# Kernel optimization log

Hardware: AMD Instinct MI355X
Metric: run time of the kernel (lower is better)

## Reference

```python
import jax, jax.numpy as jnp
import numpy as np

B, SQ, SKV, D = 4, 2048, 2048, 768
H, HD = 12, 16  # num_heads, reduced head_dim (64 / reduce_factor 4)
DR = H * HD     # 192 reduced width


def setup_inputs() -> dict:
    key = jax.random.key(0)
    ks = jax.random.split(key, 6)
    s = 0.02
    return {
        "hidden_states": jax.random.normal(ks[0], (B, SQ, D), jnp.float32),
        "encoder_hidden_states": jax.random.normal(ks[1], (B, SKV, D), jnp.float32),
        "Wq": jax.random.normal(ks[2], (D, DR), jnp.float32) * s,
        "bq": jnp.zeros((DR,), jnp.float32),
        "Wkv": jax.random.normal(ks[3], (D, 2 * DR), jnp.float32) * s,
        "bkv": jnp.zeros((2 * DR,), jnp.float32),
        "Wp": jax.random.normal(ks[4], (DR, D), jnp.float32) * s,
        "bp": jnp.zeros((D,), jnp.float32),
    }


def _split_heads(x):
    # [B, S, DR] -> [B, H, S, HD]
    b, s, _ = x.shape
    return x.reshape(b, s, H, HD).transpose(0, 2, 1, 3)


def reference(hidden_states, encoder_hidden_states, Wq, bq, Wkv, bkv, Wp, bp):
    # Conv1D projections (x @ W + b)
    q = hidden_states @ Wq + bq                       # [B, SQ, 192]
    kv = encoder_hidden_states @ Wkv + bkv            # [B, SKV, 384]
    k, v = kv[..., :DR], kv[..., DR:]
    q = _split_heads(q)                               # [B, H, SQ, HD]
    k = _split_heads(k)                               # [B, H, SKV, HD]
    v = _split_heads(v)                               # [B, H, SKV, HD]
    scale = jnp.asarray(HD, q.dtype) ** 0.5
    scores = jnp.einsum('bhqd,bhkd->bhqk', q, k) / scale
    attn = jax.nn.softmax(scores, axis=-1)            # dropout is identity in eval
    out = jnp.einsum('bhqk,bhkd->bhqd', attn, v)      # [B, H, SQ, HD]
    out = out.transpose(0, 2, 1, 3).reshape(hidden_states.shape[0], -1, DR)
    out = out @ Wp + bp                               # [B, SQ, 768]
    return out
```

## Files before the change

kernel.cpp:

```cpp
#include <hip/hip_runtime.h>
#include <hip/hip_bf16.h>
#include <math.h>

#define NB 4
#define NSQ 2048
#define NSKV 2048
#define ND 768
#define NH 12
#define NHD 16
#define NDR 192
#define M_TOT (NB * NSQ)

typedef __attribute__((ext_vector_type(8)))  short          bf16x8;
typedef __attribute__((ext_vector_type(16))) float          f32x16;
typedef __attribute__((ext_vector_type(8)))  unsigned short u16x8;

__device__ __forceinline__ unsigned short bfbits(float x) {
  __hip_bfloat16 h = __float2bfloat16(x);
  unsigned short u; __builtin_memcpy(&u, &h, 2); return u;
}
__device__ __forceinline__ float bf2f(unsigned short u) {
  unsigned int v = ((unsigned int)u) << 16; float f; __builtin_memcpy(&f, &v, 4); return f;
}
__device__ __forceinline__ unsigned int pk2t(float a, float b) {
  unsigned int ua, ub;
  __builtin_memcpy(&ua, &a, 4); __builtin_memcpy(&ub, &b, 4);
#if __has_builtin(__builtin_amdgcn_perm)
  return __builtin_amdgcn_perm(ub, ua, 0x07060302);
#else
  return (ua >> 16) | (ub & 0xffff0000u);
#endif
}
__device__ __forceinline__ float exp2_raw(float x) {
#if __has_builtin(__builtin_amdgcn_exp2f)
  return __builtin_amdgcn_exp2f(x);
#else
  float r; asm("v_exp_f32 %0, %1" : "=v"(r) : "v"(x)); return r;
#endif
}
__device__ __forceinline__ void g2l16(const void* g, void* l) {
  __builtin_amdgcn_global_load_lds(
      (const __attribute__((address_space(1))) void*)g,
      (__attribute__((address_space(3))) void*)l, 16, 0, 0);
}

#define QSCALE 0.36067376022224085f
#define LDSBUF 16384

__global__ __launch_bounds__(256) void prep(
    const float* __restrict__ Wq, const float* __restrict__ Wkv,
    const float* __restrict__ Wp,
    unsigned short* __restrict__ WSq, unsigned short* __restrict__ WSkv,
    unsigned short* __restrict__ WSp) {
  int bid = blockIdx.x;
  const float* W; unsigned short* out; int Nn, KBLK, bx, by;
  if (bid < 72)        { W = Wq;  out = WSq;  Nn = 192; KBLK = 24; bx = bid % 24;        by = bid / 24; }
  else if (bid < 216)  { int b = bid - 72;  W = Wkv; out = WSkv; Nn = 384; KBLK = 24; bx = b % 24; by = b / 24; }
  else                 { int b = bid - 216; W = Wp;  out = WSp;  Nn = 768; KBLK = 6;  bx = b % 6;  by = b / 6;  }

  __shared__ float tile[32][65];
  int k0 = bx * 32, n0 = by * 64;
  int t = threadIdx.x;
  int kr = t >> 3, c0 = (t & 7) * 8;
  const float* src = W + (size_t)(k0 + kr) * Nn + n0 + c0;
  float4 f0 = *reinterpret_cast<const float4*>(src);
  float4 f1 = *reinterpret_cast<const float4*>(src + 4);
  tile[kr][c0+0] = f0.x; tile[kr][c0+1] = f0.y; tile[kr][c0+2] = f0.z; tile[kr][c0+3] = f0.w;
  tile[kr][c0+4] = f1.x; tile[kr][c0+5] = f1.y; tile[kr][c0+6] = f1.z; tile[kr][c0+7] = f1.w;
  __syncthreads();
  int n = t >> 2, cq0 = (t & 3) * 2;
  int ng = n0 + n, sw = ng & 7;
  unsigned short* dst = out + ((size_t)ng * KBLK + bx) * 64;
  #pragma unroll
  for (int q = 0; q < 2; ++q) {
    int cc = cq0 + q;
    u16x8 v;
    #pragma unroll
    for (int i = 0; i < 8; ++i) {
      float x = tile[(cc & 3) * 8 + i][n];
      unsigned short h = bfbits(x);
      v[i] = (cc < 4) ? h : bfbits(x - bf2f(h));
    }
    *reinterpret_cast<u16x8*>(dst + (cc ^ sw) * 8) = v;
  }
}

__device__ __forceinline__ void core_compute(
    const unsigned short* const (&ard)[4], const unsigned short* const (&wrd)[12],
    int off, f32x16 (&acc)[3]) {
  #pragma unroll
  for (int kk = 0; kk < 2; ++kk) {
    bf16x8 ah = *reinterpret_cast<const bf16x8*>(ard[kk*2+0] + off);
    bf16x8 al = *reinterpret_cast<const bf16x8*>(ard[kk*2+1] + off);
    #pragma unroll
    for (int nr = 0; nr < 3; ++nr) {
      bf16x8 wh = *reinterpret_cast<const bf16x8*>(wrd[(nr*2+kk)*2+0] + off);
      bf16x8 wl = *reinterpret_cast<const bf16x8*>(wrd[(nr*2+kk)*2+1] + off);
      acc[nr] = __builtin_amdgcn_mfma_f32_32x32x16_bf16(ah, wh, acc[nr], 0, 0, 0);
      acc[nr] = __builtin_amdgcn_mfma_f32_32x32x16_bf16(ah, wl, acc[nr], 0, 0, 0);
      acc[nr] = __builtin_amdgcn_mfma_f32_32x32x16_bf16(al, wh, acc[nr], 0, 0, 0);
    }
  }
}

__device__ __forceinline__ void gemm_core(
    const unsigned short* __restrict__ As,
    const unsigned short* __restrict__ Ws,
    const float* __restrict__ bias,
    int KBLK, unsigned short* lds, f32x16 (&acc)[3]) {
  const int tid = threadIdx.x;
  const int wv = tid >> 6, lane = tid & 63;
  const int l31 = lane & 31, hi8 = lane >> 5;
  const int wm = wv >> 1, wn = wv & 1;

  unsigned short* Ab = lds;
  unsigned short* Wb = lds + 64 * 64;

  const int r8 = lane >> 3, c8 = lane & 7;
  const size_t rowu = (size_t)KBLK * 64;

  const unsigned short* srcA0 = As + (size_t)((0*4 + wv)*8 + r8) * rowu + c8*8;
  const unsigned short* srcA1 = As + (size_t)((1*4 + wv)*8 + r8) * rowu + c8*8;
  const unsigned short* srcW[6];
  #pragma unroll
  for (int j = 0; j < 6; ++j)
    srcW[j] = Ws + (size_t)((j*4 + wv)*8 + r8) * rowu + c8*8;

  unsigned short* dA0 = Ab + ((0*4 + wv)*64 + lane) * 8;
  unsigned short* dA1 = Ab + ((1*4 + wv)*64 + lane) * 8;
  unsigned short* dW[6];
  #pragma unroll
  for (int j = 0; j < 6; ++j)
    dW[j] = Wb + ((j*4 + wv)*64 + lane) * 8;

  const int ra = wm*32 + l31;
  const unsigned short* ard[4];
  #pragma unroll
  for (int kk = 0; kk < 2; ++kk) {
    ard[kk*2+0] = Ab + ra*64 + (((kk*2 + hi8)     ^ (ra & 7)) * 8);
    ard[kk*2+1] = Ab + ra*64 + (((4 + kk*2 + hi8) ^ (ra & 7)) * 8);
  }
  const unsigned short* wrd[12];
  #pragma unroll
  for (int nr = 0; nr < 3; ++nr) {
    int rw = wn*96 + nr*32 + l31;
    #pragma unroll
    for (int kk = 0; kk < 2; ++kk) {
      wrd[(nr*2+kk)*2+0] = Wb + rw*64 + (((kk*2 + hi8)     ^ (rw & 7)) * 8);
      wrd[(nr*2+kk)*2+1] = Wb + rw*64 + (((4 + kk*2 + hi8) ^ (rw & 7)) * 8);
    }
  }

  #pragma unroll
  for (int nr = 0; nr < 3; ++nr) {
    float bv = bias[wn*96 + nr*32 + l31];
    #pragma unroll
    for (int r = 0; r < 16; ++r) acc[nr][r] = bv;
  }

  g2l16(srcA0, dA0); srcA0 += 64;
  g2l16(srcA1, dA1); srcA1 += 64;
  #pragma unroll
  for (int j = 0; j < 6; ++j) { g2l16(srcW[j], dW[j]); srcW[j] += 64; }
  __syncthreads();

  for (int kb = 0; kb < KBLK; kb += 2) {
    if (kb + 1 < KBLK) {
      g2l16(srcA0, dA0 + LDSBUF); srcA0 += 64;
      g2l16(srcA1, dA1 + LDSBUF); srcA1 += 64;
      #pragma unroll
      for (int j = 0; j < 6; ++j) { g2l16(srcW[j], dW[j] + LDSBUF); srcW[j] += 64; }
    }
    core_compute(ard, wrd, 0, acc);
    __syncthreads();
    if (kb + 2 < KBLK) {
      g2l16(srcA0, dA0); srcA0 += 64;
      g2l16(srcA1, dA1); srcA1 += 64;
      #pragma unroll
      for (int j = 0; j < 6; ++j) { g2l16(srcW[j], dW[j]); srcW[j] += 64; }
    }
    core_compute(ard, wrd, LDSBUF, acc);
    __syncthreads();
  }
}

#define QHALF 10240
__global__ __launch_bounds__(384) void gemm_qkv(
    const float* __restrict__ A1, const float* __restrict__ A2,
    const unsigned short* __restrict__ WSq, const unsigned short* __restrict__ WSkv,
    const float* __restrict__ bq, const float* __restrict__ bkv,
    unsigned short* __restrict__ Qbf, unsigned short* __restrict__ Kbf,
    unsigned short* __restrict__ VTbf) {
  __shared__ unsigned short lds[2 * QHALF];
  const int bid = blockIdx.x;
  const float* Afp; const unsigned short* Ws; const float* bias;
  int m0, mode, ntile;
  if (bid < 256) {
    mode = 0; ntile = (bid & 1) * 96;
    Afp = A1; Ws = WSq + (size_t)ntile * (24*64); bias = bq + ntile;
    m0 = (bid >> 1) * 64;
  } else {
    int b2 = bid - 256;
    int sub = b2 & 3;
    m0 = (b2 >> 2) * 64;
    Afp = A2;
    if (sub < 2) { mode = 1; ntile = sub * 96;
                   Ws = WSkv + (size_t)ntile * (24*64); bias = bkv + ntile; }
    else         { mode = 2; ntile = (sub - 2) * 96;
                   Ws = WSkv + (size_t)(192 + ntile) * (24*64); bias = bkv + 192 + ntile; }
  }
  Afp += (size_t)m0 * ND;

  const int tid = threadIdx.x;
  const int wv = tid >> 6, lane = tid & 63;
  const int l31 = lane & 31, hi8 = lane >> 5;
  const int wm = wv & 1, wn = wv >> 1;

  unsigned short* Ab = lds;
  unsigned short* Wb = lds + 64*64;

  const int ar = tid >> 2, cq = tid & 3;
  const bool doA = (tid < 256);
  const float* srcA = Afp + (size_t)(doA ? ar : 0) * ND + cq*8;
  unsigned short* dAh = Ab + (doA ? ar : 0)*64 + ((cq       ^ (ar & 7)) * 8);
  unsigned short* dAl = Ab + (doA ? ar : 0)*64 + (((cq + 4) ^ (ar & 7)) * 8);

  const int wch0 = tid, wch1 = tid + 384;
  const unsigned short* srcW0 = Ws + (size_t)(wch0 >> 3) * (24*64) + (wch0 & 7) * 8;
  const unsigned short* srcW1 = Ws + (size_t)(wch1 >> 3) * (24*64) + (wch1 & 7) * 8;
  unsigned short* dW0 = Wb + wch0 * 8;
  unsigned short* dW1 = Wb + wch1 * 8;

  const int ra = wm*32 + l31;
  const int rw = wn*32 + l31;
  const unsigned short* ard[4];
  const unsigned short* wrd[4];
  #pragma unroll
  for (int kk = 0; kk < 2; ++kk) {
    ard[kk*2+0] = Ab + ra*64 + (((kk*2 + hi8)     ^ (ra & 7)) * 8);
    ard[kk*2+1] = Ab + ra*64 + (((4 + kk*2 + hi8) ^ (ra & 7)) * 8);
    wrd[kk*2+0] = Wb + rw*64 + (((kk*2 + hi8)     ^ (rw & 7)) * 8);
    wrd[kk*2+1] = Wb + rw*64 + (((4 + kk*2 + hi8) ^ (rw & 7)) * 8);
  }

  f32x16 acc;
  {
    float bv = bias[wn*32 + l31];
    #pragma unroll
    for (int r = 0; r < 16; ++r) acc[r] = bv;
  }

  {
    g2l16(srcW0, dW0); srcW0 += 64;
    g2l16(srcW1, dW1); srcW1 += 64;
    if (doA) {
      float4 f0 = *reinterpret_cast<const float4*>(srcA);
      float4 f1 = *reinterpret_cast<const float4*>(srcA + 4);
      float x[8] = {f0.x, f0.y, f0.z, f0.w, f1.x, f1.y, f1.z, f1.w};
      u16x8 hv, lv;
      #pragma unroll
      for (int i = 0; i < 8; ++i) {
        unsigned short h = bfbits(x[i]);
        hv[i] = h; lv[i] = bfbits(x[i] - bf2f(h));
      }
      *reinterpret_cast<u16x8*>(dAh) = hv;
      *reinterpret_cast<u16x8*>(dAl) = lv;
    }
    srcA += 32;
  }
  __syncthreads();

  #define QKV_COMPUTE(off)                                                     \
    {                                                                          \
      _Pragma("unroll")                                                        \
      for (int kk = 0; kk < 2; ++kk) {                                         \
        bf16x8 ah = *reinterpret_cast<const bf16x8*>(ard[kk*2+0] + (off));     \
        bf16x8 al = *reinterpret_cast<const bf16x8*>(ard[kk*2+1] + (off));     \
        bf16x8 wh = *reinterpret_cast<const bf16x8*>(wrd[kk*2+0] + (off));     \
        bf16x8 wl = *reinterpret_cast<const bf16x8*>(wrd[kk*2+1] + (off));     \
        acc = __builtin_amdgcn_mfma_f32_32x32x16_bf16(ah, wh, acc, 0, 0, 0);   \
        acc = __builtin_amdgcn_mfma_f32_32x32x16_bf16(ah, wl, acc, 0, 0, 0);   \
        acc = __builtin_amdgcn_mfma_f32_32x32x16_bf16(al, wh, acc, 0, 0, 0);   \
      }                                                                        \
    }

  for (int kb = 0; kb < 24; kb += 2) {
    float4 f0, f1;
    g2l16(srcW0, dW0 + QHALF); srcW0 += 64;
    g2l16(srcW1, dW1 + QHALF); srcW1 += 64;
    if (doA) {
      f0 = *reinterpret_cast<const float4*>(srcA);
      f1 = *reinterpret_cast<const float4*>(srcA + 4);
    }
    srcA += 32;
    QKV_COMPUTE(0)
    if (doA) {
      float x[8] = {f0.x, f0.y, f0.z, f0.w, f1.x, f1.y, f1.z, f1.w};
      u16x8 hv, lv;
      #pragma unroll
      for (int i = 0; i < 8; ++i) {
        unsigned short h = bfbits(x[i]);
        hv[i] = h; lv[i] = bfbits(x[i] - bf2f(h));
      }
      *reinterpret_cast<u16x8*>(dAh + QHALF) = hv;
      *reinterpret_cast<u16x8*>(dAl + QHALF) = lv;
    }
    __syncthreads();
    bool has2 = (kb + 2 < 24);
    if (has2) {
      g2l16(srcW0, dW0); srcW0 += 64;
      g2l16(srcW1, dW1); srcW1 += 64;
      if (doA) {
        f0 = *reinterpret_cast<const float4*>(srcA);
        f1 = *reinterpret_cast<const float4*>(srcA + 4);
      }
      srcA += 32;
    }
    QKV_COMPUTE(QHALF)
    if (has2 && doA) {
      float x[8] = {f0.x, f0.y, f0.z, f0.w, f1.x, f1.y, f1.z, f1.w};
      u16x8 hv, lv;
      #pragma unroll
      for (int i = 0; i < 8; ++i) {
        unsigned short h = bfbits(x[i]);
        hv[i] = h; lv[i] = bfbits(x[i] - bf2f(h));
      }
      *reinterpret_cast<u16x8*>(dAh) = hv;
      *reinterpret_cast<u16x8*>(dAl) = lv;
    }
    __syncthreads();
  }
  #undef QKV_COMPUTE

  if (mode == 2) {
    unsigned short (*tile)[65] = reinterpret_cast<unsigned short(*)[65]>(lds);
    #pragma unroll
    for (int r = 0; r < 16; ++r) {
      int key_l = wm*32 + (r & 3) + 8*(r >> 2) + 4*hi8;
      tile[wn*32 + l31][key_l] = bfbits(acc[r]);
    }
    __syncthreads();
    int b = m0 >> 11, key0 = m0 & 2047;
    #pragma unroll
    for (int j = 0; j < 2; ++j) {
      int flat = j * 384 + tid;
      int row = flat >> 3;
      int ck = flat & 7;
      int vcol = ntile + row;
      int h = vcol >> 4, d = vcol & 15;
      u16x8 v;
      #pragma unroll
      for (int jj = 0; jj < 8; ++jj) v[jj] = tile[row][ck*8 + jj];
      *reinterpret_cast<u16x8*>(
          &VTbf[(((size_t)(b*NH + h)*256 + (key0 >> 3) + ck)*16 + d)*8]) = v;
    }
    return;
  }

  unsigned short* outp = (mode == 0) ? Qbf : Kbf;
  const float scale = (mode == 0) ? QSCALE : 1.0f;
  {
    int col = ntile + wn*32 + l31;
    int h = col >> 4, d = col & 15;
    #pragma unroll
    for (int r = 0; r < 16; ++r) {
      int mg = m0 + wm*32 + (r & 3) + 8*(r >> 2) + 4*hi8;
      int b = mg >> 11, q = mg & 2047;
      outp[(((size_t)b*NH + h)*NSQ + q)*16 + d] = bfbits(acc[r] * scale);
    }
  }
}

__device__ __forceinline__ void attn_tile32(
    bf16x8 qf, bf16x8 kf, bf16x8 vf0, bf16x8 vf1,
    int hi8, const f32x16& zeroc, f32x16& acc) {
  f32x16 s = __builtin_amdgcn_mfma_f32_32x32x16_bf16(kf, qf, zeroc, 0, 0, 0);

  float p[16];
  #pragma unroll
  for (int r = 0; r < 16; ++r) p[r] = exp2_raw(s[r]);

  unsigned int w[8];
  #pragma unroll
  for (int t8 = 0; t8 < 8; ++t8) w[t8] = pk2t(p[2*t8], p[2*t8+1]);

  unsigned int t0 = hi8 ? w[0] : w[2], t1 = hi8 ? w[1] : w[3];
  unsigned int t2 = hi8 ? w[4] : w[6], t3 = hi8 ? w[5] : w[7];
  unsigned int r0 = (unsigned int)__shfl_xor((int)t0, 32);
  unsigned int r1 = (unsigned int)__shfl_xor((int)t1, 32);
  unsigned int r2 = (unsigned int)__shfl_xor((int)t2, 32);
  unsigned int r3 = (unsigned int)__shfl_xor((int)t3, 32);

  union { bf16x8 v; unsigned int u[4]; } pa0, pa1;
  pa0.u[0] = hi8 ? r0 : w[0];  pa0.u[1] = hi8 ? r1 : w[1];
  pa0.u[2] = hi8 ? w[2] : r0;  pa0.u[3] = hi8 ? w[3] : r1;
  pa1.u[0] = hi8 ? r2 : w[4];  pa1.u[1] = hi8 ? r3 : w[5];
  pa1.u[2] = hi8 ? w[6] : r2;  pa1.u[3] = hi8 ? w[7] : r3;

  __builtin_amdgcn_s_setprio(1);
  acc = __builtin_amdgcn_mfma_f32_32x32x16_bf16(vf0, pa0.v, acc, 0, 0, 0);
  acc = __builtin_amdgcn_mfma_f32_32x32x16_bf16(vf1, pa1.v, acc, 0, 0, 0);
  __builtin_amdgcn_s_setprio(0);
}

__global__ __launch_bounds__(256, 4) void attn_bf16(
    const unsigned short* __restrict__ Qbf, const unsigned short* __restrict__ Kbf,
    const unsigned short* __restrict__ VT, unsigned short* __restrict__ AOS) {
  __shared__ float comb[4][64][9];
  const int tid = threadIdx.x;
  const int wave = tid >> 6, lane = tid & 63;
  const int l31 = lane & 31, hi8 = lane >> 5;
  const int bid = blockIdx.x;
  const int qt = bid & 63;
  const int bh = bid >> 6;
  const int q = qt * 32 + l31;

  bf16x8 qf = *reinterpret_cast<const bf16x8*>(&Qbf[((size_t)bh*NSQ + q)*16 + hi8*8]);
  const unsigned short* kbase = Kbf + (size_t)bh * NSKV * 16;

  const short fillv = (l31 == 16) ? (short)0x3F80 : (short)0;
  bf16x8 vfill;
  #pragma unroll
  for (int j = 0; j < 8; ++j) vfill[j] = fillv;

  f32x16 acc;
  #pragma unroll
  for (int r = 0; r < 16; ++r) acc[r] = 0.f;
  const f32x16 zeroc = acc;

  const int kstart = wave * (NSKV / 4);
  const unsigned short* kp = &kbase[(size_t)(kstart + l31)*16 + hi8*8];
  const unsigned short* vwave = VT + ((((size_t)bh*256 + (kstart >> 3) + hi8)*16 + l31) * 8);

  bf16x8 k0, v00, v10;
  bf16x8 k1, v01, v11;

  k0  = *reinterpret_cast<const bf16x8*>(kp);
  v00 = vfill; v10 = vfill;
  if (l31 < 16) {
    v00 = *reinterpret_cast<const bf16x8*>(vwave);
    v10 = *reinterpret_cast<const bf16x8*>(vwave + 256);
  }

  for (int kt = 0; kt < 512; kt += 64) {
    {
      k1 = *reinterpret_cast<const bf16x8*>(kp + (size_t)(kt + 32) * 16);
      v01 = vfill; v11 = vfill;
      if (l31 < 16) {
        const unsigned short* vq = vwave + (size_t)(kt + 32) * 16;
        v01 = *reinterpret_cast<const bf16x8*>(vq);
        v11 = *reinterpret_cast<const bf16x8*>(vq + 256);
      }
    }
    attn_tile32(qf, k0, v00, v10, hi8, zeroc, acc);
    if (kt + 64 < 512) {
      k0 = *reinterpret_cast<const bf16x8*>(kp + (size_t)(kt + 64) * 16);
      v00 = vfill; v10 = vfill;
      if (l31 < 16) {
        const unsigned short* vq = vwave + (size_t)(kt + 64) * 16;
        v00 = *reinterpret_cast<const bf16x8*>(vq);
        v10 = *reinterpret_cast<const bf16x8*>(vq + 256);
      }
    }
    attn_tile32(qf, k1, v01, v11, hi8, zeroc, acc);
  }

  {
    float* cb = &comb[wave][lane][0];
    #pragma unroll
    for (int r = 0; r < 9; ++r) cb[r] = acc[r];
  }
  __syncthreads();

  if (wave == 0) {
    float A[9];
    #pragma unroll
    for (int r = 0; r < 9; ++r)
      A[r] = ((comb[0][lane][r] + comb[1][lane][r]) +
              (comb[2][lane][r] + comb[3][lane][r]));
    float L = A[8] + __shfl_xor(A[8], 32);
    float inv = 1.f / L;

    unsigned short oh[8], ol[8];
    #pragma unroll
    for (int r = 0; r < 8; ++r) {
      float o = A[r] * inv;
      oh[r] = bfbits(o);
      ol[r] = bfbits(o - bf2f(oh[r]));
    }
    int b = bh / NH, h = bh % NH;
    int mrow = b * NSQ + q;
    unsigned short* rowp = AOS + (size_t)mrow * (6 * 64);
    int sw = mrow & 7;
    int kblk = h >> 1;
    int cA = (h & 1) * 2;
    unsigned short* p0;
    p0 = rowp + ((kblk*8 + ((cA + 0) ^ sw)) * 8) + 4*hi8;
    reinterpret_cast<unsigned int*>(p0)[0] = (unsigned)oh[0] | ((unsigned)oh[1] << 16);
    reinterpret_cast<unsigned int*>(p0)[1] = (unsigned)oh[2] | ((unsigned)oh[3] << 16);
    p0 = rowp + ((kblk*8 + ((cA + 1) ^ sw)) * 8) + 4*hi8;
    reinterpret_cast<unsigned int*>(p0)[0] = (unsigned)oh[4] | ((unsigned)oh[5] << 16);
    reinterpret_cast<unsigned int*>(p0)[1] = (unsigned)oh[6] | ((unsigned)oh[7] << 16);
    p0 = rowp + ((kblk*8 + ((cA + 4) ^ sw)) * 8) + 4*hi8;
    reinterpret_cast<unsigned int*>(p0)[0] = (unsigned)ol[0] | ((unsigned)ol[1] << 16);
    reinterpret_cast<unsigned int*>(p0)[1] = (unsigned)ol[2] | ((unsigned)ol[3] << 16);
    p0 = rowp + ((kblk*8 + ((cA + 5) ^ sw)) * 8) + 4*hi8;
    reinterpret_cast<unsigned int*>(p0)[0] = (unsigned)ol[4] | ((unsigned)ol[5] << 16);
    reinterpret_cast<unsigned int*>(p0)[1] = (unsigned)ol[6] | ((unsigned)ol[7] << 16);
  }
}

__global__ __launch_bounds__(256) void gemm_out_k(
    const unsigned short* __restrict__ AOS, const unsigned short* __restrict__ WSp,
    const float* __restrict__ bp, float* __restrict__ out) {
  __shared__ unsigned short lds[2 * LDSBUF];
  const int bid = blockIdx.x;
  const int KBLK = NDR / 32;
  int m0 = (bid >> 2) * 64;
  int n0 = (bid & 3) * 192;
  const unsigned short* As = AOS + (size_t)m0 * KBLK * 64;
  const unsigned short* Ws = WSp + (size_t)n0 * KBLK * 64;
  f32x16 acc[3];
  gemm_core(As, Ws, bp + n0, KBLK, lds, acc);

  const int tid = threadIdx.x;
  const int wv = tid >> 6, lane = tid & 63;
  const int l31 = lane & 31, hi8 = lane >> 5;
  const int wm = wv >> 1, wn = wv & 1;
  #pragma unroll
  for (int nr = 0; nr < 3; ++nr) {
    int n = n0 + wn*96 + nr*32 + l31;
    #pragma unroll
    for (int r = 0; r < 16; ++r) {
      int mg = m0 + wm*32 + (r & 3) + 8*(r >> 2) + 4*hi8;
      out[(size_t)mg * ND + n] = acc[nr][r];
    }
  }
}

extern "C" void kernel_launch(void* const* d_in, const int* in_sizes, int n_in,
                              void* d_out, int out_size, void* d_ws, size_t ws_size,
                              hipStream_t stream) {
  const float* hs  = (const float*)d_in[0];
  const float* ehs = (const float*)d_in[1];
  const float* Wq  = (const float*)d_in[2];
  const float* bq  = (const float*)d_in[3];
  const float* Wkv = (const float*)d_in[4];
  const float* bkv = (const float*)d_in[5];
  const float* Wp  = (const float*)d_in[6];
  const float* bp  = (const float*)d_in[7];
  float* out = (float*)d_out;

  char* w = (char*)d_ws;
  unsigned short* AOS = (unsigned short*)w;
  char* w2 = w + (size_t)M_TOT * 6 * 64 * 2;
  unsigned short* WSq  = (unsigned short*)w2;
  unsigned short* WSkv = (unsigned short*)(w2 + 589824);
  unsigned short* WSp  = (unsigned short*)(w2 + 589824 + 1179648);
  char* w3 = w2 + 589824 + 1179648 + 589824;
  unsigned short* Qbf  = (unsigned short*)w3;
  unsigned short* Kbf  = Qbf + (size_t)M_TOT * NDR;
  unsigned short* VTbf = Kbf + (size_t)M_TOT * NDR;

  prep<<<dim3(72 + 144 + 72), dim3(256), 0, stream>>>(
      Wq, Wkv, Wp, WSq, WSkv, WSp);
  gemm_qkv<<<dim3(768), dim3(384), 0, stream>>>(hs, ehs, WSq, WSkv, bq, bkv, Qbf, Kbf, VTbf);
  attn_bf16<<<dim3(NB * NH * 64), dim3(256), 0, stream>>>(Qbf, Kbf, VTbf, AOS);
  gemm_out_k<<<dim3(512), dim3(256), 0, stream>>>(AOS, WSp, bp, out);
}
```

Before: 89.08 us.

## Pre-split activations into MFMA fragment layout and load QKV operands directly to registers

The fp32-to-bf16 hi/lo split of hidden and encoder states moves out of the QKV GEMM into the prep kernel, which writes A and W in a fragment-ready layout. The QKV GEMM then drops LDS staging and barriers, loads bf16x8 fragments straight from global into registers with double buffering, and switches to 64x64 tiles with 256 threads over more blocks. The goal is to remove in-loop conversion, LDS traffic and sync stalls. The cost is an extra global write and read of the split activations (about 2x the fp32 input bytes as bf16 hi/lo) and reliance on cache for reuse of A across the N tiles.

```diff
diff --git a/kernel.cpp b/kernel.cpp
--- a/kernel.cpp
+++ b/kernel.cpp
@@ -47,30 +47,57 @@
 #define QSCALE 0.36067376022224085f
 #define LDSBUF 16384
 
-__global__ __launch_bounds__(256) void prep(
+__global__ __launch_bounds__(256) void prep_all(
     const float* __restrict__ Wq, const float* __restrict__ Wkv,
     const float* __restrict__ Wp,
-    unsigned short* __restrict__ WSq, unsigned short* __restrict__ WSkv,
-    unsigned short* __restrict__ WSp) {
+    const float* __restrict__ hs, const float* __restrict__ ehs,
+    unsigned short* __restrict__ WS2q, unsigned short* __restrict__ WS2kv,
+    unsigned short* __restrict__ WSp,
+    unsigned short* __restrict__ AT1, unsigned short* __restrict__ AT2) {
   int bid = blockIdx.x;
-  const float* W; unsigned short* out; int Nn, KBLK, bx, by;
-  if (bid < 72)        { W = Wq;  out = WSq;  Nn = 192; KBLK = 24; bx = bid % 24;        by = bid / 24; }
-  else if (bid < 216)  { int b = bid - 72;  W = Wkv; out = WSkv; Nn = 384; KBLK = 24; bx = b % 24; by = b / 24; }
-  else                 { int b = bid - 216; W = Wp;  out = WSp;  Nn = 768; KBLK = 6;  bx = b % 6;  by = b / 6;  }
+  const int tid = threadIdx.x;
+
+  if (bid >= 288) {
+    int b2 = bid - 288;
+    const float* A = (b2 < 128) ? hs : ehs;
+    unsigned short* AT = (b2 < 128) ? AT1 : AT2;
+    int mt = b2 & 127;
+    int r = tid & 63, cq = tid >> 6;
+    const float* s = A + (size_t)(mt*64 + r) * ND + cq*8;
+    unsigned short* dst = AT + (size_t)mt*24*4096 + cq*512 + r*8;
+    #pragma unroll 2
+    for (int kb = 0; kb < 24; ++kb) {
+      float4 f0 = *reinterpret_cast<const float4*>(s + kb*32);
+      float4 f1 = *reinterpret_cast<const float4*>(s + kb*32 + 4);
+      float x[8] = {f0.x, f0.y, f0.z, f0.w, f1.x, f1.y, f1.z, f1.w};
+      u16x8 hv, lv;
+      #pragma unroll
+      for (int i = 0; i < 8; ++i) {
+        unsigned short h = bfbits(x[i]);
+        hv[i] = h; lv[i] = bfbits(x[i] - bf2f(h));
+      }
+      *reinterpret_cast<u16x8*>(dst + kb*4096)        = hv;
+      *reinterpret_cast<u16x8*>(dst + kb*4096 + 2048) = lv;
+    }
+    return;
+  }
+
+  const float* W; unsigned short* out; int Nn, KBLK, bx, by; bool oldlay;
+  if (bid < 72)       { W = Wq;  out = WS2q;  Nn = 192; KBLK = 24; bx = bid % 24;      by = bid / 24; oldlay = false; }
+  else if (bid < 216) { int b = bid - 72;  W = Wkv; out = WS2kv; Nn = 384; KBLK = 24; bx = b % 24; by = b / 24; oldlay = false; }
+  else                { int b = bid - 216; W = Wp;  out = WSp;   Nn = 768; KBLK = 6;  bx = b % 6;  by = b / 6;  oldlay = true; }
 
   __shared__ float tile[32][65];
   int k0 = bx * 32, n0 = by * 64;
-  int t = threadIdx.x;
-  int kr = t >> 3, c0 = (t & 7) * 8;
+  int kr = tid >> 3, c0 = (tid & 7) * 8;
   const float* src = W + (size_t)(k0 + kr) * Nn + n0 + c0;
   float4 f0 = *reinterpret_cast<const float4*>(src);
   float4 f1 = *reinterpret_cast<const float4*>(src + 4);
   tile[kr][c0+0] = f0.x; tile[kr][c0+1] = f0.y; tile[kr][c0+2] = f0.z; tile[kr][c0+3] = f0.w;
   tile[kr][c0+4] = f1.x; tile[kr][c0+5] = f1.y; tile[kr][c0+6] = f1.z; tile[kr][c0+7] = f1.w;
   __syncthreads();
-  int n = t >> 2, cq0 = (t & 3) * 2;
+  int n = tid >> 2, cq0 = (tid & 3) * 2;
   int ng = n0 + n, sw = ng & 7;
-  unsigned short* dst = out + ((size_t)ng * KBLK + bx) * 64;
   #pragma unroll
   for (int q = 0; q < 2; ++q) {
     int cc = cq0 + q;
@@ -81,7 +108,13 @@
       unsigned short h = bfbits(x);
       v[i] = (cc < 4) ? h : bfbits(x - bf2f(h));
     }
-    *reinterpret_cast<u16x8*>(dst + (cc ^ sw) * 8) = v;
+    if (oldlay) {
+      unsigned short* dst = out + ((size_t)ng * KBLK + bx) * 64;
+      *reinterpret_cast<u16x8*>(dst + (cc ^ sw) * 8) = v;
+    } else {
+      *reinterpret_cast<u16x8*>(
+          out + ((((size_t)by * KBLK + bx) * 8 + cc) * 64 + n) * 8) = v;
+    }
   }
 }
 
@@ -184,64 +217,34 @@
   }
 }
 
-#define QHALF 10240
-__global__ __launch_bounds__(384) void gemm_qkv(
-    const float* __restrict__ A1, const float* __restrict__ A2,
-    const unsigned short* __restrict__ WSq, const unsigned short* __restrict__ WSkv,
+__global__ __launch_bounds__(256, 4) void gemm_qkv(
+    const unsigned short* __restrict__ AT1, const unsigned short* __restrict__ AT2,
+    const unsigned short* __restrict__ WS2q, const unsigned short* __restrict__ WS2kv,
     const float* __restrict__ bq, const float* __restrict__ bkv,
     unsigned short* __restrict__ Qbf, unsigned short* __restrict__ Kbf,
     unsigned short* __restrict__ VTbf) {
-  __shared__ unsigned short lds[2 * QHALF];
+  __shared__ unsigned short vt_tile[64][65];
   const int bid = blockIdx.x;
-  const float* Afp; const unsigned short* Ws; const float* bias;
-  int m0, mode, ntile;
-  if (bid < 256) {
-    mode = 0; ntile = (bid & 1) * 96;
-    Afp = A1; Ws = WSq + (size_t)ntile * (24*64); bias = bq + ntile;
-    m0 = (bid >> 1) * 64;
-  } else {
-    int b2 = bid - 256;
-    int sub = b2 & 3;
-    m0 = (b2 >> 2) * 64;
-    Afp = A2;
-    if (sub < 2) { mode = 1; ntile = sub * 96;
-                   Ws = WSkv + (size_t)ntile * (24*64); bias = bkv + ntile; }
-    else         { mode = 2; ntile = (sub - 2) * 96;
-                   Ws = WSkv + (size_t)(192 + ntile) * (24*64); bias = bkv + 192 + ntile; }
-  }
-  Afp += (size_t)m0 * ND;
+  const int mt = bid / 9, nt = bid % 9;
+  const int m0 = mt * 64;
+
+  const unsigned short* AT; const unsigned short* Wbase; const float* bias;
+  int mode, ncol0;
+  if (nt < 3)      { mode = 0; AT = AT1; Wbase = WS2q  + (size_t)nt*98304;
+                     ncol0 = nt*64;        bias = bq + ncol0; }
+  else if (nt < 6) { mode = 1; AT = AT2; Wbase = WS2kv + (size_t)(nt-3)*98304;
+                     ncol0 = (nt-3)*64;    bias = bkv + ncol0; }
+  else             { mode = 2; AT = AT2; Wbase = WS2kv + (size_t)(nt-3)*98304;
+                     ncol0 = (nt-6)*64;    bias = bkv + 192 + ncol0; }
 
   const int tid = threadIdx.x;
   const int wv = tid >> 6, lane = tid & 63;
   const int l31 = lane & 31, hi8 = lane >> 5;
-  const int wm = wv & 1, wn = wv >> 1;
-
-  unsigned short* Ab = lds;
-  unsigned short* Wb = lds + 64*64;
-
-  const int ar = tid >> 2, cq = tid & 3;
-  const bool doA = (tid < 256);
-  const float* srcA = Afp + (size_t)(doA ? ar : 0) * ND + cq*8;
-  unsigned short* dAh = Ab + (doA ? ar : 0)*64 + ((cq       ^ (ar & 7)) * 8);
-  unsigned short* dAl = Ab + (doA ? ar : 0)*64 + (((cq + 4) ^ (ar & 7)) * 8);
-
-  const int wch0 = tid, wch1 = tid + 384;
-  const unsigned short* srcW0 = Ws + (size_t)(wch0 >> 3) * (24*64) + (wch0 & 7) * 8;
-  const unsigned short* srcW1 = Ws + (size_t)(wch1 >> 3) * (24*64) + (wch1 & 7) * 8;
-  unsigned short* dW0 = Wb + wch0 * 8;
-  unsigned short* dW1 = Wb + wch1 * 8;
-
-  const int ra = wm*32 + l31;
-  const int rw = wn*32 + l31;
-  const unsigned short* ard[4];
-  const unsigned short* wrd[4];
-  #pragma unroll
-  for (int kk = 0; kk < 2; ++kk) {
-    ard[kk*2+0] = Ab + ra*64 + (((kk*2 + hi8)     ^ (ra & 7)) * 8);
-    ard[kk*2+1] = Ab + ra*64 + (((4 + kk*2 + hi8) ^ (ra & 7)) * 8);
-    wrd[kk*2+0] = Wb + rw*64 + (((kk*2 + hi8)     ^ (rw & 7)) * 8);
-    wrd[kk*2+1] = Wb + rw*64 + (((4 + kk*2 + hi8) ^ (rw & 7)) * 8);
-  }
+  const int wm = wv >> 1, wn = wv & 1;
+
+  const unsigned short* pA = AT + (size_t)mt*24*4096 + (size_t)hi8*512
+                                + (size_t)(wm*32 + l31)*8;
+  const unsigned short* pW = Wbase + (size_t)hi8*512 + (size_t)(wn*32 + l31)*8;
 
   f32x16 acc;
   {
@@ -250,107 +253,64 @@
     for (int r = 0; r < 16; ++r) acc[r] = bv;
   }
 
-  {
-    g2l16(srcW0, dW0); srcW0 += 64;
-    g2l16(srcW1, dW1); srcW1 += 64;
-    if (doA) {
-      float4 f0 = *reinterpret_cast<const float4*>(srcA);
-      float4 f1 = *reinterpret_cast<const float4*>(srcA + 4);
-      float x[8] = {f0.x, f0.y, f0.z, f0.w, f1.x, f1.y, f1.z, f1.w};
-      u16x8 hv, lv;
-      #pragma unroll
-      for (int i = 0; i < 8; ++i) {
-        unsigned short h = bfbits(x[i]);
-        hv[i] = h; lv[i] = bfbits(x[i] - bf2f(h));
-      }
-      *reinterpret_cast<u16x8*>(dAh) = hv;
-      *reinterpret_cast<u16x8*>(dAl) = lv;
-    }
-    srcA += 32;
-  }
-  __syncthreads();
-
-  #define QKV_COMPUTE(off)                                                     \
-    {                                                                          \
-      _Pragma("unroll")                                                        \
-      for (int kk = 0; kk < 2; ++kk) {                                         \
-        bf16x8 ah = *reinterpret_cast<const bf16x8*>(ard[kk*2+0] + (off));     \
-        bf16x8 al = *reinterpret_cast<const bf16x8*>(ard[kk*2+1] + (off));     \
-        bf16x8 wh = *reinterpret_cast<const bf16x8*>(wrd[kk*2+0] + (off));     \
-        bf16x8 wl = *reinterpret_cast<const bf16x8*>(wrd[kk*2+1] + (off));     \
-        acc = __builtin_amdgcn_mfma_f32_32x32x16_bf16(ah, wh, acc, 0, 0, 0);   \
-        acc = __builtin_amdgcn_mfma_f32_32x32x16_bf16(ah, wl, acc, 0, 0, 0);   \
-        acc = __builtin_amdgcn_mfma_f32_32x32x16_bf16(al, wh, acc, 0, 0, 0);   \
-      }                                                                        \
-    }
+  bf16x8 a0h0, a0h1, a0l0, a0l1, w0h0, w0h1, w0l0, w0l1;
+  bf16x8 a1h0, a1h1, a1l0, a1l1, w1h0, w1h1, w1l0, w1l1;
+
+  #define LD(p) (*reinterpret_cast<const bf16x8*>(p))
+  a0h0 = LD(pA);        a0h1 = LD(pA + 1024);
+  a0l0 = LD(pA + 2048); a0l1 = LD(pA + 3072);
+  w0h0 = LD(pW);        w0h1 = LD(pW + 1024);
+  w0l0 = LD(pW + 2048); w0l1 = LD(pW + 3072);
+
+  #define COMPUTE(ah0_, ah1_, al0_, al1_, wh0_, wh1_, wl0_, wl1_)              \
+    acc = __builtin_amdgcn_mfma_f32_32x32x16_bf16(ah0_, wh0_, acc, 0, 0, 0);   \
+    acc = __builtin_amdgcn_mfma_f32_32x32x16_bf16(ah0_, wl0_, acc, 0, 0, 0);   \
+    acc = __builtin_amdgcn_mfma_f32_32x32x16_bf16(al0_, wh0_, acc, 0, 0, 0);   \
+    acc = __builtin_amdgcn_mfma_f32_32x32x16_bf16(ah1_, wh1_, acc, 0, 0, 0);   \
+    acc = __builtin_amdgcn_mfma_f32_32x32x16_bf16(ah1_, wl1_, acc, 0, 0, 0);   \
+    acc = __builtin_amdgcn_mfma_f32_32x32x16_bf16(al1_, wh1_, acc, 0, 0, 0);
 
   for (int kb = 0; kb < 24; kb += 2) {
-    float4 f0, f1;
-    g2l16(srcW0, dW0 + QHALF); srcW0 += 64;
-    g2l16(srcW1, dW1 + QHALF); srcW1 += 64;
-    if (doA) {
-      f0 = *reinterpret_cast<const float4*>(srcA);
-      f1 = *reinterpret_cast<const float4*>(srcA + 4);
-    }
-    srcA += 32;
-    QKV_COMPUTE(0)
-    if (doA) {
-      float x[8] = {f0.x, f0.y, f0.z, f0.w, f1.x, f1.y, f1.z, f1.w};
-      u16x8 hv, lv;
-      #pragma unroll
-      for (int i = 0; i < 8; ++i) {
-        unsigned short h = bfbits(x[i]);
-        hv[i] = h; lv[i] = bfbits(x[i] - bf2f(h));
-      }
-      *reinterpret_cast<u16x8*>(dAh + QHALF) = hv;
-      *reinterpret_cast<u16x8*>(dAl + QHALF) = lv;
-    }
-    __syncthreads();
-    bool has2 = (kb + 2 < 24);
-    if (has2) {
-      g2l16(srcW0, dW0); srcW0 += 64;
-      g2l16(srcW1, dW1); srcW1 += 64;
-      if (doA) {
-        f0 = *reinterpret_cast<const float4*>(srcA);
-        f1 = *reinterpret_cast<const float4*>(srcA + 4);
-      }
-      srcA += 32;
-    }
-    QKV_COMPUTE(QHALF)
-    if (has2 && doA) {
-      float x[8] = {f0.x, f0.y, f0.z, f0.w, f1.x, f1.y, f1.z, f1.w};
-      u16x8 hv, lv;
-      #pragma unroll
-      for (int i = 0; i < 8; ++i) {
-        unsigned short h = bfbits(x[i]);
-        hv[i] = h; lv[i] = bfbits(x[i] - bf2f(h));
-      }
-      *reinterpret_cast<u16x8*>(dAh) = hv;
-      *reinterpret_cast<u16x8*>(dAl) = lv;
-    }
-    __syncthreads();
-  }
-  #undef QKV_COMPUTE
+    {
+      const unsigned short* qa = pA + (size_t)(kb + 1)*4096;
+      const unsigned short* qw = pW + (size_t)(kb + 1)*4096;
+      a1h0 = LD(qa);        a1h1 = LD(qa + 1024);
+      a1l0 = LD(qa + 2048); a1l1 = LD(qa + 3072);
+      w1h0 = LD(qw);        w1h1 = LD(qw + 1024);
+      w1l0 = LD(qw + 2048); w1l1 = LD(qw + 3072);
+    }
+    COMPUTE(a0h0, a0h1, a0l0, a0l1, w0h0, w0h1, w0l0, w0l1)
+    if (kb + 2 < 24) {
+      const unsigned short* qa = pA + (size_t)(kb + 2)*4096;
+      const unsigned short* qw = pW + (size_t)(kb + 2)*4096;
+      a0h0 = LD(qa);        a0h1 = LD(qa + 1024);
+      a0l0 = LD(qa + 2048); a0l1 = LD(qa + 3072);
+      w0h0 = LD(qw);        w0h1 = LD(qw + 1024);
+      w0l0 = LD(qw + 2048); w0l1 = LD(qw + 3072);
+    }
+    COMPUTE(a1h0, a1h1, a1l0, a1l1, w1h0, w1h1, w1l0, w1l1)
+  }
+  #undef COMPUTE
+  #undef LD
 
   if (mode == 2) {
-    unsigned short (*tile)[65] = reinterpret_cast<unsigned short(*)[65]>(lds);
     #pragma unroll
     for (int r = 0; r < 16; ++r) {
       int key_l = wm*32 + (r & 3) + 8*(r >> 2) + 4*hi8;
-      tile[wn*32 + l31][key_l] = bfbits(acc[r]);
+      vt_tile[wn*32 + l31][key_l] = bfbits(acc[r]);
     }
     __syncthreads();
     int b = m0 >> 11, key0 = m0 & 2047;
     #pragma unroll
     for (int j = 0; j < 2; ++j) {
-      int flat = j * 384 + tid;
+      int flat = j * 256 + tid;
       int row = flat >> 3;
       int ck = flat & 7;
-      int vcol = ntile + row;
+      int vcol = ncol0 + row;
       int h = vcol >> 4, d = vcol & 15;
       u16x8 v;
       #pragma unroll
-      for (int jj = 0; jj < 8; ++jj) v[jj] = tile[row][ck*8 + jj];
+      for (int jj = 0; jj < 8; ++jj) v[jj] = vt_tile[row][ck*8 + jj];
       *reinterpret_cast<u16x8*>(
           &VTbf[(((size_t)(b*NH + h)*256 + (key0 >> 3) + ck)*16 + d)*8]) = v;
     }
@@ -360,7 +320,7 @@
   unsigned short* outp = (mode == 0) ? Qbf : Kbf;
   const float scale = (mode == 0) ? QSCALE : 1.0f;
   {
-    int col = ntile + wn*32 + l31;
+    int col = ncol0 + wn*32 + l31;
     int h = col >> 4, d = col & 15;
     #pragma unroll
     for (int r = 0; r < 16; ++r) {
@@ -552,19 +512,22 @@
   float* out = (float*)d_out;
 
   char* w = (char*)d_ws;
+  unsigned short* AT1 = (unsigned short*)w;
   unsigned short* AOS = (unsigned short*)w;
-  char* w2 = w + (size_t)M_TOT * 6 * 64 * 2;
-  unsigned short* WSq  = (unsigned short*)w2;
-  unsigned short* WSkv = (unsigned short*)(w2 + 589824);
-  unsigned short* WSp  = (unsigned short*)(w2 + 589824 + 1179648);
-  char* w3 = w2 + 589824 + 1179648 + 589824;
+  unsigned short* AT2 = AT1 + (size_t)128*24*4096;
+  char* w2 = (char*)(AT2 + (size_t)128*24*4096);
+  unsigned short* WSp   = (unsigned short*)w2;
+  unsigned short* WS2q  = (unsigned short*)(w2 + 589824);
+  unsigned short* WS2kv = (unsigned short*)(w2 + 2*589824);
+  char* w3 = w2 + 2*589824 + 1179648;
   unsigned short* Qbf  = (unsigned short*)w3;
   unsigned short* Kbf  = Qbf + (size_t)M_TOT * NDR;
   unsigned short* VTbf = Kbf + (size_t)M_TOT * NDR;
 
-  prep<<<dim3(72 + 144 + 72), dim3(256), 0, stream>>>(
-      Wq, Wkv, Wp, WSq, WSkv, WSp);
-  gemm_qkv<<<dim3(768), dim3(384), 0, stream>>>(hs, ehs, WSq, WSkv, bq, bkv, Qbf, Kbf, VTbf);
+  prep_all<<<dim3(544), dim3(256), 0, stream>>>(
+      Wq, Wkv, Wp, hs, ehs, WS2q, WS2kv, WSp, AT1, AT2);
+  gemm_qkv<<<dim3(128 * 9), dim3(256), 0, stream>>>(
+      AT1, AT2, WS2q, WS2kv, bq, bkv, Qbf, Kbf, VTbf);
   attn_bf16<<<dim3(NB * NH * 64), dim3(256), 0, stream>>>(Qbf, Kbf, VTbf, AOS);
   gemm_out_k<<<dim3(512), dim3(256), 0, stream>>>(AOS, WSp, bp, out);
 }
```

After: 111.6 us. +25.2%, slower.
